# Performance work log

Measured on AMD Instinct MI355X. Metric: run time of the kernel, lower is better.

## Reference

```python
import jax, jax.numpy as jnp
import numpy as np

B, S, H, HS, D = 256, 16, 8, 128, 1024
M = H * HS  # mem_size = 1024
FORGET_BIAS = 1.0


def setup_inputs() -> dict:
    key = jax.random.key(0)
    ks = jax.random.split(key, 16)
    n = lambda k, shape, s=0.02: (jax.random.normal(k, shape, jnp.float32) * s)
    return {
        'inputs': jax.random.normal(ks[0], (B, D), jnp.float32),
        'h_state': jax.random.normal(ks[1], (B, S, M), jnp.float32),
        'm_state': jax.random.normal(ks[2], (B, S, M), jnp.float32),
        'W_emb': n(ks[3], (D, M)), 'b_emb': jnp.zeros((M,), jnp.float32),
        'W_g': n(ks[4], (M, M)), 'b_g': jnp.zeros((M,), jnp.float32),
        'W_wf': n(ks[5], (D, M)), 'W_wi': n(ks[6], (D, M)), 'W_wo': n(ks[7], (D, M)),
        'W_uf': n(ks[8], (M, M)), 'b_uf': jnp.zeros((M,), jnp.float32),
        'W_ui': n(ks[9], (M, M)), 'b_ui': jnp.zeros((M,), jnp.float32),
        'W_uo': n(ks[10], (M, M)), 'b_uo': jnp.zeros((M,), jnp.float32),
    }


def _rmc_forward(inputs, h_state, m_state, W_emb, b_emb, W_g, b_g,
                 W_wf, W_wi, W_wo, W_uf, b_uf, W_ui, b_ui, W_uo, b_uo):
    # input embedding: [B, D] -> [B, M]
    dense_inputs = inputs @ W_emb + b_emb
    # keys/values: memory with the embedded input appended as an extra slot -> [B, S+1, M]
    kv = jnp.concatenate([m_state, dense_inputs[:, None, :]], axis=1)
    # multi-head scaled dot-product attention (no q/k/v projections in AttentionMap)
    q = m_state.reshape(B, S, H, HS)
    k = kv.reshape(B, S + 1, H, HS)
    v = kv.reshape(B, S + 1, H, HS)
    scores = jnp.einsum('bqhd,bkhd->bhqk', q, k) / jnp.sqrt(jnp.asarray(HS, q.dtype))
    attn = jax.nn.softmax(scores, axis=-1)
    attended = jnp.einsum('bhqk,bkhd->bqhd', attn, v).reshape(B, S, M)

    memory_proposal = m_state + attended
    memory_proposal = (memory_proposal @ W_g + b_g) + memory_proposal

    forget_gate = jax.nn.sigmoid(h_state @ W_uf + b_uf + (inputs @ W_wf)[:, None, :])
    input_gate = jax.nn.sigmoid(h_state @ W_ui + b_ui + (inputs @ W_wi)[:, None, :])
    output_gate = jax.nn.sigmoid(h_state @ W_uo + b_uo + (inputs @ W_wo)[:, None, :])

    # NOTE: faithful to the original (including the sigmoid around m*f + bias and
    # the double-sigmoid on the input/output gates)
    new_memories = jax.nn.sigmoid(m_state * forget_gate + FORGET_BIAS) \
        + memory_proposal * jax.nn.sigmoid(input_gate)
    new_hidden = jnp.tanh(m_state) * jax.nn.sigmoid(output_gate)
    return new_memories, new_hidden


def reference(inputs, h_state, m_state, W_emb, b_emb, W_g, b_g,
              W_wf, W_wi, W_wo, W_uf, b_uf, W_ui, b_ui, W_uo, b_uo):
    return _rmc_forward(inputs, h_state, m_state, W_emb, b_emb, W_g, b_g,
                        W_wf, W_wi, W_wo, W_uf, b_uf, W_ui, b_ui, W_uo, b_uo)
```

## Files before the change

### kernel.cpp

```cpp
#include <hip/hip_runtime.h>
#include <hip/hip_bf16.h>


typedef __hip_bfloat16 bf16;
typedef __bf16 bf16x8 __attribute__((ext_vector_type(8)));
typedef float  f32x4  __attribute__((ext_vector_type(4)));

__device__ __forceinline__ float b2f(bf16 x) { return __bfloat162float(x); }
__device__ __forceinline__ bf16  f2b(float x) { return __float2bfloat16(x); }
__device__ __forceinline__ float sig(float x) { return 1.0f / (1.0f + __expf(-x)); }

__device__ __forceinline__ void gl_lds16(const void* g, void* l) {
    __builtin_amdgcn_global_load_lds(
        (const __attribute__((address_space(1))) void*)g,
        (__attribute__((address_space(3))) void*)l,
        16, 0, 0);
}

__device__ __forceinline__ float4 ld_bf4(const bf16* p) {
    ushort4 u = *(const ushort4*)p;
    float4 r;
    r.x = b2f(*(const bf16*)&u.x);
    r.y = b2f(*(const bf16*)&u.y);
    r.z = b2f(*(const bf16*)&u.z);
    r.w = b2f(*(const bf16*)&u.w);
    return r;
}

__global__ __launch_bounds__(256) void k_prep(
    const float* __restrict__ W0, const float* __restrict__ W1,
    const float* __restrict__ W2, const float* __restrict__ W3,
    const float* __restrict__ W4, const float* __restrict__ W5,
    const float* __restrict__ W6, const float* __restrict__ W7,
    const float* __restrict__ h_state, const float* __restrict__ inputs,
    bf16* __restrict__ wt, bf16* __restrict__ hbf, bf16* __restrict__ xbf)
{
    const int blk = blockIdx.x;
    const int tid = threadIdx.x;

    if (blk < 8192) {
        const float* Ws[8] = {W0, W1, W2, W3, W4, W5, W6, W7};
        const int plane = blk >> 10;
        const int t = blk & 1023;
        const int nb = (t & 31) * 32, kb = (t >> 5) * 32;
        const float* W = Ws[plane];
        bf16* Wt = wt + (size_t)plane * (1024 * 1024);

        __shared__ float tl[32][33];
        const int tx = tid & 31, ty = tid >> 5;

        #pragma unroll
        for (int r = 0; r < 4; ++r)
            tl[r * 8 + ty][tx] = W[(size_t)(kb + r * 8 + ty) * 1024 + nb + tx];
        __syncthreads();
        #pragma unroll
        for (int r = 0; r < 4; ++r)
            Wt[(size_t)(nb + r * 8 + ty) * 1024 + kb + tx] = f2b(tl[tx][r * 8 + ty]);
    } else if (blk < 10240) {
        const int e = blk - 8192;
        int idx = (e * 256 + tid) * 8;
        #pragma unroll
        for (int half = 0; half < 2; ++half) {
            float4 v = *(const float4*)(h_state + idx + half * 4);
            hbf[idx + half * 4 + 0] = f2b(v.x);
            hbf[idx + half * 4 + 1] = f2b(v.y);
            hbf[idx + half * 4 + 2] = f2b(v.z);
            hbf[idx + half * 4 + 3] = f2b(v.w);
        }
    } else {
        const int e = blk - 10240;
        int idx = (e * 256 + tid) * 8;
        #pragma unroll
        for (int half = 0; half < 2; ++half) {
            float4 v = *(const float4*)(inputs + idx + half * 4);
            xbf[idx + half * 4 + 0] = f2b(v.x);
            xbf[idx + half * 4 + 1] = f2b(v.y);
            xbf[idx + half * 4 + 2] = f2b(v.z);
            xbf[idx + half * 4 + 3] = f2b(v.w);
        }
    }
}

__global__ __launch_bounds__(256) void k_gemm1(
    const bf16* __restrict__ hbf,
    const bf16* __restrict__ xbf,
    const bf16* __restrict__ wt,
    const float* __restrict__ b_emb,
    bf16* __restrict__ pre,
    float* __restrict__ proj)
{
    __shared__ __align__(16) char smem[32768];

    const int bid = blockIdx.x;
    const int wv = threadIdx.x >> 6;
    const int lane = threadIdx.x & 63;
    const int r8 = lane >> 3, c8 = lane & 7;
    const int mrow = lane & 15, q = lane >> 4;

    const bf16* A;
    int m0, plane, bn0;
    if (bid < 768) {
        int bx = bid % 24, by = bid / 24;
        A = hbf; m0 = by * 128;
        int n0g = bx * 128;
        plane = 1 + (n0g >> 10); bn0 = n0g & 1023;
    } else {
        int e = bid - 768;
        int bx = e & 31, by = e >> 5;
        A = xbf; m0 = by * 128;
        int n0x = bx * 128;
        plane = 4 + (n0x >> 10); bn0 = n0x & 1023;
    }
    const bf16* Bp = wt + (size_t)plane * (1024 * 1024);

    const f32x4 zero4 = {0.0f, 0.0f, 0.0f, 0.0f};
    f32x4 acc[4][4];
    #pragma unroll
    for (int i = 0; i < 4; ++i)
        #pragma unroll
        for (int j = 0; j < 4; ++j) acc[i][j] = zero4;

    const int rb = (wv & 1) * 64, cb = (wv >> 1) * 64;

    for (int k0 = 0; k0 < 1024; k0 += 64) {
        #pragma unroll
        for (int t = 0; t < 4; ++t) {
            int rr = wv * 32 + t * 8;
            gl_lds16(A  + (size_t)(m0  + rr + r8) * 1024 + k0 + c8 * 8, smem + rr * 128);
            gl_lds16(Bp + (size_t)(bn0 + rr + r8) * 1024 + k0 + c8 * 8, smem + 16384 + rr * 128);
        }
        __syncthreads();

        #pragma unroll
        for (int kk = 0; kk < 2; ++kk) {
            const int kb = kk * 64 + q * 16;
            bf16x8 a[4], b[4];
            #pragma unroll
            for (int i = 0; i < 4; ++i)
                a[i] = *(const bf16x8*)(smem + (rb + i * 16 + mrow) * 128 + kb);
            #pragma unroll
            for (int j = 0; j < 4; ++j)
                b[j] = *(const bf16x8*)(smem + 16384 + (cb + j * 16 + mrow) * 128 + kb);
            #pragma unroll
            for (int i = 0; i < 4; ++i)
                #pragma unroll
                for (int j = 0; j < 4; ++j)
                    acc[i][j] = __builtin_amdgcn_mfma_f32_16x16x32_bf16(a[i], b[j], acc[i][j], 0, 0, 0);
        }
        __syncthreads();
    }

    if (bid < 768) {
        bf16* P = pre + (size_t)(plane - 1) * (4096 * 1024);
        #pragma unroll
        for (int j = 0; j < 4; ++j) {
            const int colp = bn0 + cb + j * 16 + mrow;
            #pragma unroll
            for (int i = 0; i < 4; ++i)
                #pragma unroll
                for (int r = 0; r < 4; ++r) {
                    const int row = m0 + rb + i * 16 + q * 4 + r;
                    P[(size_t)row * 1024 + colp] = f2b(acc[i][j][r]);
                }
        }
    } else {
        const int which = plane - 4;
        float* P = proj + which * 262144;
        #pragma unroll
        for (int j = 0; j < 4; ++j) {
            const int colp = bn0 + cb + j * 16 + mrow;
            const float bias = (which == 0) ? b_emb[colp] : 0.0f;
            #pragma unroll
            for (int i = 0; i < 4; ++i)
                #pragma unroll
                for (int r = 0; r < 4; ++r) {
                    const int row = m0 + rb + i * 16 + q * 4 + r;
                    P[(size_t)row * 1024 + colp] = acc[i][j][r] + bias;
                }
        }
    }
}

__global__ __launch_bounds__(256) void k_attn(
    const float* __restrict__ m_state,
    const float* __restrict__ dense,
    bf16* __restrict__ mp)
{
    const int b = blockIdx.x >> 3;
    const int h = blockIdx.x & 7;
    const int tid = threadIdx.x;

    __shared__ float kv[17][132];
    __shared__ float sc[16][18];

    for (int idx = tid; idx < 17 * 32; idx += 256) {
        int r = idx >> 5, d4 = idx & 31;
        const float* src = (r < 16)
            ? &m_state[(size_t)(b * 16 + r) * 1024 + h * 128 + d4 * 4]
            : &dense[(size_t)b * 1024 + h * 128 + d4 * 4];
        float4 v = *(const float4*)src;
        *(float4*)&kv[r][d4 * 4] = v;
    }
    __syncthreads();

    for (int p = tid; p < 16 * 17; p += 256) {
        int qi = p / 17, ki = p % 17;
        float dx = 0.f, dy = 0.f, dz = 0.f, dw = 0.f;
        #pragma unroll 8
        for (int d4 = 0; d4 < 32; ++d4) {
            float4 a = *(const float4*)&kv[qi][d4 * 4];
            float4 c = *(const float4*)&kv[ki][d4 * 4];
            dx += a.x * c.x; dy += a.y * c.y; dz += a.z * c.z; dw += a.w * c.w;
        }
        sc[qi][ki] = (dx + dy + dz + dw) * 0.0883883476483184f;
    }
    __syncthreads();

    if (tid < 16) {
        float mx = -1e30f;
        for (int k = 0; k < 17; ++k) mx = fmaxf(mx, sc[tid][k]);
        float s = 0.0f;
        for (int k = 0; k < 17; ++k) { float e = __expf(sc[tid][k] - mx); sc[tid][k] = e; s += e; }
        float inv = 1.0f / s;
        for (int k = 0; k < 17; ++k) sc[tid][k] *= inv;
    }
    __syncthreads();

    for (int p = tid; p < 16 * 32; p += 256) {
        int qi = p >> 5, d4 = p & 31;
        float sx = 0.f, sy = 0.f, sz = 0.f, sw = 0.f;
        #pragma unroll
        for (int k = 0; k < 17; ++k) {
            float w = sc[qi][k];
            float4 v = *(const float4*)&kv[k][d4 * 4];
            sx += w * v.x; sy += w * v.y; sz += w * v.z; sw += w * v.w;
        }
        float4 base = *(const float4*)&kv[qi][d4 * 4];
        size_t off = (size_t)(b * 16 + qi) * 1024 + h * 128 + d4 * 4;
        mp[off + 0] = f2b(base.x + sx);
        mp[off + 1] = f2b(base.y + sy);
        mp[off + 2] = f2b(base.z + sz);
        mp[off + 3] = f2b(base.w + sw);
    }
}

__global__ __launch_bounds__(256) void k_gemm2(
    const bf16* __restrict__ mpb,
    const bf16* __restrict__ wtg,
    bf16* __restrict__ preg)
{
    __shared__ __align__(16) char smem[24576];

    const int m0 = (blockIdx.x >> 3) * 64;
    const int n0 = (blockIdx.x & 7) * 128;
    const int wv = threadIdx.x >> 6;
    const int lane = threadIdx.x & 63;
    const int r8 = lane >> 3, c8 = lane & 7;
    const int mrow = lane & 15, q = lane >> 4;

    const f32x4 zero4 = {0.0f, 0.0f, 0.0f, 0.0f};
    f32x4 acc[2][4];
    #pragma unroll
    for (int i = 0; i < 2; ++i)
        #pragma unroll
        for (int j = 0; j < 4; ++j) acc[i][j] = zero4;

    const int rb = (wv & 1) * 32, cb = (wv >> 1) * 64;

    for (int k0 = 0; k0 < 1024; k0 += 64) {
        #pragma unroll
        for (int t = 0; t < 2; ++t) {
            int rr = wv * 16 + t * 8;
            gl_lds16(mpb + (size_t)(m0 + rr + r8) * 1024 + k0 + c8 * 8, smem + rr * 128);
        }
        #pragma unroll
        for (int t = 0; t < 4; ++t) {
            int rr = wv * 32 + t * 8;
            gl_lds16(wtg + (size_t)(n0 + rr + r8) * 1024 + k0 + c8 * 8, smem + 8192 + rr * 128);
        }
        __syncthreads();

        #pragma unroll
        for (int kk = 0; kk < 2; ++kk) {
            const int kb = kk * 64 + q * 16;
            bf16x8 a[2], b[4];
            #pragma unroll
            for (int i = 0; i < 2; ++i)
                a[i] = *(const bf16x8*)(smem + (rb + i * 16 + mrow) * 128 + kb);
            #pragma unroll
            for (int j = 0; j < 4; ++j)
                b[j] = *(const bf16x8*)(smem + 8192 + (cb + j * 16 + mrow) * 128 + kb);
            #pragma unroll
            for (int i = 0; i < 2; ++i)
                #pragma unroll
                for (int j = 0; j < 4; ++j)
                    acc[i][j] = __builtin_amdgcn_mfma_f32_16x16x32_bf16(a[i], b[j], acc[i][j], 0, 0, 0);
        }
        __syncthreads();
    }

    #pragma unroll
    for (int j = 0; j < 4; ++j) {
        const int col = n0 + cb + j * 16 + mrow;
        #pragma unroll
        for (int i = 0; i < 2; ++i)
            #pragma unroll
            for (int r = 0; r < 4; ++r) {
                const int row = m0 + rb + i * 16 + q * 4 + r;
                preg[(size_t)row * 1024 + col] = f2b(acc[i][j][r]);
            }
    }
}

__global__ __launch_bounds__(256) void k_epi(
    const float* __restrict__ m_state,
    const bf16* __restrict__ mpb,
    const bf16* __restrict__ preg,
    const bf16* __restrict__ pre,
    const float* __restrict__ proj,
    const float* __restrict__ b_g, const float* __restrict__ b_uf,
    const float* __restrict__ b_ui, const float* __restrict__ b_uo,
    float* __restrict__ out_mem, float* __restrict__ out_hid)
{
    const int idx = (blockIdx.x * 256 + threadIdx.x) * 4;
    const int row = idx >> 10;
    const int col = idx & 1023;
    const int b = row >> 4;

    float4 m4  = *(const float4*)(m_state + idx);
    float4 mp4 = ld_bf4(mpb + idx);
    float4 pg4 = ld_bf4(preg + idx);
    float4 pf4 = ld_bf4(pre + idx);
    float4 pi4 = ld_bf4(pre + 4194304 + idx);
    float4 po4 = ld_bf4(pre + 8388608 + idx);
    float4 xf4 = *(const float4*)(proj + 262144 + b * 1024 + col);
    float4 xi4 = *(const float4*)(proj + 524288 + b * 1024 + col);
    float4 xo4 = *(const float4*)(proj + 786432 + b * 1024 + col);
    float4 bg4 = *(const float4*)(b_g + col);
    float4 bf4 = *(const float4*)(b_uf + col);
    float4 bi4 = *(const float4*)(b_ui + col);
    float4 bo4 = *(const float4*)(b_uo + col);

    float4 om, oh;
    {
        float mp2 = pg4.x + bg4.x + mp4.x;
        float fg = sig(pf4.x + bf4.x + xf4.x);
        float ig = sig(pi4.x + bi4.x + xi4.x);
        float og = sig(po4.x + bo4.x + xo4.x);
        om.x = sig(m4.x * fg + 1.0f) + mp2 * sig(ig);
        oh.x = tanhf(m4.x) * sig(og);
    }
    {
        float mp2 = pg4.y + bg4.y + mp4.y;
        float fg = sig(pf4.y + bf4.y + xf4.y);
        float ig = sig(pi4.y + bi4.y + xi4.y);
        float og = sig(po4.y + bo4.y + xo4.y);
        om.y = sig(m4.y * fg + 1.0f) + mp2 * sig(ig);
        oh.y = tanhf(m4.y) * sig(og);
    }
    {
        float mp2 = pg4.z + bg4.z + mp4.z;
        float fg = sig(pf4.z + bf4.z + xf4.z);
        float ig = sig(pi4.z + bi4.z + xi4.z);
        float og = sig(po4.z + bo4.z + xo4.z);
        om.z = sig(m4.z * fg + 1.0f) + mp2 * sig(ig);
        oh.z = tanhf(m4.z) * sig(og);
    }
    {
        float mp2 = pg4.w + bg4.w + mp4.w;
        float fg = sig(pf4.w + bf4.w + xf4.w);
        float ig = sig(pi4.w + bi4.w + xi4.w);
        float og = sig(po4.w + bo4.w + xo4.w);
        om.w = sig(m4.w * fg + 1.0f) + mp2 * sig(ig);
        oh.w = tanhf(m4.w) * sig(og);
    }

    *(float4*)(out_mem + idx) = om;
    *(float4*)(out_hid + idx) = oh;
}

extern "C" void kernel_launch(void* const* d_in, const int* in_sizes, int n_in,
                              void* d_out, int out_size, void* d_ws, size_t ws_size,
                              hipStream_t stream)
{
    const float* inputs  = (const float*)d_in[0];
    const float* h_state = (const float*)d_in[1];
    const float* m_state = (const float*)d_in[2];
    const float* W_emb   = (const float*)d_in[3];
    const float* b_emb   = (const float*)d_in[4];
    const float* W_g     = (const float*)d_in[5];
    const float* b_g     = (const float*)d_in[6];
    const float* W_wf    = (const float*)d_in[7];
    const float* W_wi    = (const float*)d_in[8];
    const float* W_wo    = (const float*)d_in[9];
    const float* W_uf    = (const float*)d_in[10];
    const float* b_uf    = (const float*)d_in[11];
    const float* W_ui    = (const float*)d_in[12];
    const float* b_ui    = (const float*)d_in[13];
    const float* W_uo    = (const float*)d_in[14];
    const float* b_uo    = (const float*)d_in[15];

    char* wsb = (char*)d_ws;
    float* proj = (float*)wsb;
    bf16*  hmp  = (bf16*)(wsb + 4u  * 1048576u);
    bf16*  wt   = (bf16*)(wsb + 12u * 1048576u);
    bf16*  xbf  = (bf16*)(wsb + 28u * 1048576u);
    bf16*  pre  = (bf16*)(wsb + 29u * 1048576u);
    bf16*  preg = (bf16*)(wsb + 20u * 1048576u);

    float* out_mem = (float*)d_out;
    float* out_hid = out_mem + (size_t)4096 * 1024;

    k_prep<<<dim3(10368), dim3(256), 0, stream>>>(
        W_g, W_uf, W_ui, W_uo, W_emb, W_wf, W_wi, W_wo,
        h_state, inputs, wt, hmp, xbf);

    k_gemm1<<<dim3(832), dim3(256), 0, stream>>>(
        hmp, xbf, wt, b_emb, pre, proj);

    k_attn<<<dim3(256 * 8), dim3(256), 0, stream>>>(m_state, proj, hmp);

    k_gemm2<<<dim3(512), dim3(256), 0, stream>>>(hmp, wt, preg);

    k_epi<<<dim3(4096), dim3(256), 0, stream>>>(
        m_state, hmp, preg, pre, proj,
        b_g, b_uf, b_ui, b_uo, out_mem, out_hid);
}
```

Measured before the change: 239.2 us.

## Fuse input projections into prep and merge gate and proposal GEMMs into one pipelined kernel

The small input-side projections (emb, wf, wi, wo) now run inside k_prep, converting fp32 inputs and weights to bf16 on the fly, so neither the xbf buffer nor the transposed copies of those four weights are needed. The three h_state gate GEMMs and the memory-proposal GEMM become one 256x256-tile, 512-thread kernel with double-buffered LDS, XOR-swizzled layout and explicit waitcnt/barrier pipelining, run after attention. The separate gemm1 launch goes away. tanhf is swapped for an exp-based approximation. The cost is 128KB of dynamic LDS, a grid of only 256 blocks, and a serial K loop over only 64 blocks for the projection GEMM inside prep.

Measured after the change: 233.9 us. 1.02x faster.

```diff
diff --git a/kernel.cpp b/kernel.cpp
--- a/kernel.cpp
+++ b/kernel.cpp
@@ -8,7 +8,14 @@
 
 __device__ __forceinline__ float b2f(bf16 x) { return __bfloat162float(x); }
 __device__ __forceinline__ bf16  f2b(float x) { return __float2bfloat16(x); }
+__device__ __forceinline__ unsigned short fbits(float x) {
+    bf16 b = __float2bfloat16(x);
+    return *(unsigned short*)&b;
+}
 __device__ __forceinline__ float sig(float x) { return 1.0f / (1.0f + __expf(-x)); }
+__device__ __forceinline__ float ftanh(float x) {
+    return 1.0f - 2.0f / (1.0f + __expf(2.0f * x));
+}
 
 __device__ __forceinline__ void gl_lds16(const void* g, void* l) {
     __builtin_amdgcn_global_load_lds(
@@ -28,36 +35,126 @@
 }
 
 __global__ __launch_bounds__(256) void k_prep(
-    const float* __restrict__ W0, const float* __restrict__ W1,
-    const float* __restrict__ W2, const float* __restrict__ W3,
-    const float* __restrict__ W4, const float* __restrict__ W5,
-    const float* __restrict__ W6, const float* __restrict__ W7,
+    const float* __restrict__ W_g, const float* __restrict__ W_uf,
+    const float* __restrict__ W_ui, const float* __restrict__ W_uo,
+    const float* __restrict__ W_emb, const float* __restrict__ W_wf,
+    const float* __restrict__ W_wi, const float* __restrict__ W_wo,
+    const float* __restrict__ b_emb,
     const float* __restrict__ h_state, const float* __restrict__ inputs,
-    bf16* __restrict__ wt, bf16* __restrict__ hbf, bf16* __restrict__ xbf)
+    bf16* __restrict__ wt, bf16* __restrict__ hbf, float* __restrict__ proj)
 {
+    __shared__ __align__(16) char sbuf[32768];
     const int blk = blockIdx.x;
     const int tid = threadIdx.x;
 
-    if (blk < 8192) {
-        const float* Ws[8] = {W0, W1, W2, W3, W4, W5, W6, W7};
-        const int plane = blk >> 10;
-        const int t = blk & 1023;
-        const int nb = (t & 31) * 32, kb = (t >> 5) * 32;
+    if (blk < 64) {
+        const float* Wsrc4[4] = {W_emb, W_wf, W_wi, W_wo};
+        const int by = blk >> 5, bx = blk & 31;
+        const int which = bx >> 3;
+        const int n0 = (bx & 7) * 128;
+        const int m0 = by * 128;
+        const float* Wsrc = Wsrc4[which];
+        char* LA = sbuf;
+        char* LB = sbuf + 16384;
+
+        const int wv = tid >> 6, lane = tid & 63;
+        const int mrow = lane & 15, q = lane >> 4;
+        const int rb = (wv & 1) * 64, cb = (wv >> 1) * 64;
+
+        const f32x4 zero4 = {0.0f, 0.0f, 0.0f, 0.0f};
+        f32x4 acc[4][4];
+        #pragma unroll
+        for (int i = 0; i < 4; ++i)
+            #pragma unroll
+            for (int j = 0; j < 4; ++j) acc[i][j] = zero4;
+
+        for (int k0 = 0; k0 < 1024; k0 += 64) {
+            #pragma unroll
+            for (int r = 0; r < 8; ++r) {
+                int lin = r * 256 + tid;
+                int row = lin >> 4, f4 = lin & 15;
+                float4 v = *(const float4*)(inputs + (size_t)(m0 + row) * 1024 + k0 + f4 * 4);
+                ushort4 p;
+                p.x = fbits(v.x); p.y = fbits(v.y); p.z = fbits(v.z); p.w = fbits(v.w);
+                *(ushort4*)(LA + row * 128 + ((f4 * 8) ^ ((row & 7) << 4))) = p;
+            }
+            #pragma unroll
+            for (int r = 0; r < 2; ++r) {
+                int lin = r * 256 + tid;
+                int kq = lin >> 5, cq = lin & 31;
+                const float* wp = Wsrc + (size_t)(k0 + kq * 4) * 1024 + n0 + cq * 4;
+                float4 v0 = *(const float4*)(wp);
+                float4 v1 = *(const float4*)(wp + 1024);
+                float4 v2 = *(const float4*)(wp + 2048);
+                float4 v3 = *(const float4*)(wp + 3072);
+                const float* e0 = (const float*)&v0;
+                const float* e1 = (const float*)&v1;
+                const float* e2 = (const float*)&v2;
+                const float* e3 = (const float*)&v3;
+                #pragma unroll
+                for (int j = 0; j < 4; ++j) {
+                    int c = cq * 4 + j;
+                    ushort4 p;
+                    p.x = fbits(e0[j]); p.y = fbits(e1[j]);
+                    p.z = fbits(e2[j]); p.w = fbits(e3[j]);
+                    *(ushort4*)(LB + c * 128 + ((kq * 8) ^ ((c & 7) << 4))) = p;
+                }
+            }
+            __syncthreads();
+            #pragma unroll
+            for (int kk = 0; kk < 2; ++kk) {
+                const int kb = kk * 64 + q * 16;
+                bf16x8 afr[4], bfr[4];
+                #pragma unroll
+                for (int i = 0; i < 4; ++i) {
+                    int row = rb + i * 16 + mrow;
+                    afr[i] = *(const bf16x8*)(LA + row * 128 + (kb ^ ((row & 7) << 4)));
+                }
+                #pragma unroll
+                for (int j = 0; j < 4; ++j) {
+                    int n = cb + j * 16 + mrow;
+                    bfr[j] = *(const bf16x8*)(LB + n * 128 + (kb ^ ((n & 7) << 4)));
+                }
+                #pragma unroll
+                for (int i = 0; i < 4; ++i)
+                    #pragma unroll
+                    for (int j = 0; j < 4; ++j)
+                        acc[i][j] = __builtin_amdgcn_mfma_f32_16x16x32_bf16(afr[i], bfr[j], acc[i][j], 0, 0, 0);
+            }
+            __syncthreads();
+        }
+        float* P = proj + which * 262144;
+        #pragma unroll
+        for (int j = 0; j < 4; ++j) {
+            const int colp = n0 + cb + j * 16 + mrow;
+            const float bias = (which == 0) ? b_emb[colp] : 0.0f;
+            #pragma unroll
+            for (int i = 0; i < 4; ++i)
+                #pragma unroll
+                for (int r = 0; r < 4; ++r) {
+                    const int row = m0 + rb + i * 16 + q * 4 + r;
+                    P[(size_t)row * 1024 + colp] = acc[i][j][r] + bias;
+                }
+        }
+    } else if (blk < 4160) {
+        const float* Ws[4] = {W_g, W_uf, W_ui, W_uo};
+        const int t = blk - 64;
+        const int plane = t >> 10;
+        const int tt = t & 1023;
+        const int nb = (tt & 31) * 32, kb2 = (tt >> 5) * 32;
         const float* W = Ws[plane];
         bf16* Wt = wt + (size_t)plane * (1024 * 1024);
-
-        __shared__ float tl[32][33];
+        float (*tl)[33] = (float (*)[33])sbuf;
         const int tx = tid & 31, ty = tid >> 5;
-
         #pragma unroll
         for (int r = 0; r < 4; ++r)
-            tl[r * 8 + ty][tx] = W[(size_t)(kb + r * 8 + ty) * 1024 + nb + tx];
+            tl[r * 8 + ty][tx] = W[(size_t)(kb2 + r * 8 + ty) * 1024 + nb + tx];
         __syncthreads();
         #pragma unroll
         for (int r = 0; r < 4; ++r)
-            Wt[(size_t)(nb + r * 8 + ty) * 1024 + kb + tx] = f2b(tl[tx][r * 8 + ty]);
-    } else if (blk < 10240) {
-        const int e = blk - 8192;
+            Wt[(size_t)(nb + r * 8 + ty) * 1024 + kb2 + tx] = f2b(tl[tx][r * 8 + ty]);
+    } else {
+        const int e = blk - 4160;
         int idx = (e * 256 + tid) * 8;
         #pragma unroll
         for (int half = 0; half < 2; ++half) {
@@ -66,117 +163,6 @@
             hbf[idx + half * 4 + 1] = f2b(v.y);
             hbf[idx + half * 4 + 2] = f2b(v.z);
             hbf[idx + half * 4 + 3] = f2b(v.w);
-        }
-    } else {
-        const int e = blk - 10240;
-        int idx = (e * 256 + tid) * 8;
-        #pragma unroll
-        for (int half = 0; half < 2; ++half) {
-            float4 v = *(const float4*)(inputs + idx + half * 4);
-            xbf[idx + half * 4 + 0] = f2b(v.x);
-            xbf[idx + half * 4 + 1] = f2b(v.y);
-            xbf[idx + half * 4 + 2] = f2b(v.z);
-            xbf[idx + half * 4 + 3] = f2b(v.w);
-        }
-    }
-}
-
-__global__ __launch_bounds__(256) void k_gemm1(
-    const bf16* __restrict__ hbf,
-    const bf16* __restrict__ xbf,
-    const bf16* __restrict__ wt,
-    const float* __restrict__ b_emb,
-    bf16* __restrict__ pre,
-    float* __restrict__ proj)
-{
-    __shared__ __align__(16) char smem[32768];
-
-    const int bid = blockIdx.x;
-    const int wv = threadIdx.x >> 6;
-    const int lane = threadIdx.x & 63;
-    const int r8 = lane >> 3, c8 = lane & 7;
-    const int mrow = lane & 15, q = lane >> 4;
-
-    const bf16* A;
-    int m0, plane, bn0;
-    if (bid < 768) {
-        int bx = bid % 24, by = bid / 24;
-        A = hbf; m0 = by * 128;
-        int n0g = bx * 128;
-        plane = 1 + (n0g >> 10); bn0 = n0g & 1023;
-    } else {
-        int e = bid - 768;
-        int bx = e & 31, by = e >> 5;
-        A = xbf; m0 = by * 128;
-        int n0x = bx * 128;
-        plane = 4 + (n0x >> 10); bn0 = n0x & 1023;
-    }
-    const bf16* Bp = wt + (size_t)plane * (1024 * 1024);
-
-    const f32x4 zero4 = {0.0f, 0.0f, 0.0f, 0.0f};
-    f32x4 acc[4][4];
-    #pragma unroll
-    for (int i = 0; i < 4; ++i)
-        #pragma unroll
-        for (int j = 0; j < 4; ++j) acc[i][j] = zero4;
-
-    const int rb = (wv & 1) * 64, cb = (wv >> 1) * 64;
-
-    for (int k0 = 0; k0 < 1024; k0 += 64) {
-        #pragma unroll
-        for (int t = 0; t < 4; ++t) {
-            int rr = wv * 32 + t * 8;
-            gl_lds16(A  + (size_t)(m0  + rr + r8) * 1024 + k0 + c8 * 8, smem + rr * 128);
-            gl_lds16(Bp + (size_t)(bn0 + rr + r8) * 1024 + k0 + c8 * 8, smem + 16384 + rr * 128);
-        }
-        __syncthreads();
-
-        #pragma unroll
-        for (int kk = 0; kk < 2; ++kk) {
-            const int kb = kk * 64 + q * 16;
-            bf16x8 a[4], b[4];
-            #pragma unroll
-            for (int i = 0; i < 4; ++i)
-                a[i] = *(const bf16x8*)(smem + (rb + i * 16 + mrow) * 128 + kb);
-            #pragma unroll
-            for (int j = 0; j < 4; ++j)
-                b[j] = *(const bf16x8*)(smem + 16384 + (cb + j * 16 + mrow) * 128 + kb);
-            #pragma unroll
-            for (int i = 0; i < 4; ++i)
-                #pragma unroll
-                for (int j = 0; j < 4; ++j)
-                    acc[i][j] = __builtin_amdgcn_mfma_f32_16x16x32_bf16(a[i], b[j], acc[i][j], 0, 0, 0);
-        }
-        __syncthreads();
-    }
-
-    if (bid < 768) {
-        bf16* P = pre + (size_t)(plane - 1) * (4096 * 1024);
-        #pragma unroll
-        for (int j = 0; j < 4; ++j) {
-            const int colp = bn0 + cb + j * 16 + mrow;
-            #pragma unroll
-            for (int i = 0; i < 4; ++i)
-                #pragma unroll
-                for (int r = 0; r < 4; ++r) {
-                    const int row = m0 + rb + i * 16 + q * 4 + r;
-                    P[(size_t)row * 1024 + colp] = f2b(acc[i][j][r]);
-                }
-        }
-    } else {
-        const int which = plane - 4;
-        float* P = proj + which * 262144;
-        #pragma unroll
-        for (int j = 0; j < 4; ++j) {
-            const int colp = bn0 + cb + j * 16 + mrow;
-            const float bias = (which == 0) ? b_emb[colp] : 0.0f;
-            #pragma unroll
-            for (int i = 0; i < 4; ++i)
-                #pragma unroll
-                for (int r = 0; r < 4; ++r) {
-                    const int row = m0 + rb + i * 16 + q * 4 + r;
-                    P[(size_t)row * 1024 + colp] = acc[i][j][r] + bias;
-                }
         }
     }
 }
@@ -244,70 +230,108 @@
     }
 }
 
-__global__ __launch_bounds__(256) void k_gemm2(
+__global__ __launch_bounds__(512, 2) void k_gemm_big(
+    const bf16* __restrict__ hbf,
     const bf16* __restrict__ mpb,
-    const bf16* __restrict__ wtg,
+    const bf16* __restrict__ wt,
+    bf16* __restrict__ pre,
     bf16* __restrict__ preg)
 {
-    __shared__ __align__(16) char smem[24576];
-
-    const int m0 = (blockIdx.x >> 3) * 64;
-    const int n0 = (blockIdx.x & 7) * 128;
+    extern __shared__ __align__(16) char smem[];
+
+    int bid = blockIdx.x;
+    bid = (bid & 7) * 32 + (bid >> 3);
+    const int by = bid & 15;
+    const int ct = bid >> 4;
+    const int m0 = by * 256;
+
+    const bf16* A; const bf16* Bp; bf16* Cout; int bn0;
+    if (ct < 12) {
+        A = hbf;
+        const int g = ct >> 2;
+        bn0 = (ct & 3) * 256;
+        Bp = wt + (size_t)(1 + g) * (1024 * 1024);
+        Cout = pre + (size_t)g * (4096 * 1024);
+    } else {
+        A = mpb;
+        bn0 = (ct - 12) * 256;
+        Bp = wt;
+        Cout = preg;
+    }
+
     const int wv = threadIdx.x >> 6;
     const int lane = threadIdx.x & 63;
     const int r8 = lane >> 3, c8 = lane & 7;
     const int mrow = lane & 15, q = lane >> 4;
+    const int wr = wv >> 2, wc = wv & 3;
 
     const f32x4 zero4 = {0.0f, 0.0f, 0.0f, 0.0f};
-    f32x4 acc[2][4];
+    f32x4 acc[8][4];
     #pragma unroll
-    for (int i = 0; i < 2; ++i)
+    for (int i = 0; i < 8; ++i)
         #pragma unroll
         for (int j = 0; j < 4; ++j) acc[i][j] = zero4;
 
-    const int rb = (wv & 1) * 32, cb = (wv >> 1) * 64;
-
-    for (int k0 = 0; k0 < 1024; k0 += 64) {
-        #pragma unroll
-        for (int t = 0; t < 2; ++t) {
-            int rr = wv * 16 + t * 8;
-            gl_lds16(mpb + (size_t)(m0 + rr + r8) * 1024 + k0 + c8 * 8, smem + rr * 128);
-        }
+    auto STAGE = [&](int buf, int k0) {
+        char* sA = smem + buf * 65536;
+        char* sB = sA + 32768;
         #pragma unroll
         for (int t = 0; t < 4; ++t) {
-            int rr = wv * 32 + t * 8;
-            gl_lds16(wtg + (size_t)(n0 + rr + r8) * 1024 + k0 + c8 * 8, smem + 8192 + rr * 128);
-        }
-        __syncthreads();
-
+            const int rr = wv * 32 + t * 8;
+            gl_lds16(A  + (size_t)(m0  + rr + r8) * 1024 + k0 + (c8 ^ r8) * 8, sA + rr * 128);
+            gl_lds16(Bp + (size_t)(bn0 + rr + r8) * 1024 + k0 + (c8 ^ r8) * 8, sB + rr * 128);
+        }
+    };
+
+    STAGE(0, 0);
+
+    #pragma unroll 2
+    for (int step = 0; step < 16; ++step) {
+        const int cur = step & 1;
+        if (step < 15) {
+            STAGE(cur ^ 1, (step + 1) * 64);
+            asm volatile("s_waitcnt vmcnt(8)" ::: "memory");
+        } else {
+            asm volatile("s_waitcnt vmcnt(0)" ::: "memory");
+        }
+        __builtin_amdgcn_s_barrier();
+        __builtin_amdgcn_sched_barrier(0);
+
+        const char* sA = smem + cur * 65536;
+        const char* sB = sA + 32768;
         #pragma unroll
         for (int kk = 0; kk < 2; ++kk) {
             const int kb = kk * 64 + q * 16;
-            bf16x8 a[2], b[4];
-            #pragma unroll
-            for (int i = 0; i < 2; ++i)
-                a[i] = *(const bf16x8*)(smem + (rb + i * 16 + mrow) * 128 + kb);
-            #pragma unroll
-            for (int j = 0; j < 4; ++j)
-                b[j] = *(const bf16x8*)(smem + 8192 + (cb + j * 16 + mrow) * 128 + kb);
-            #pragma unroll
-            for (int i = 0; i < 2; ++i)
+            bf16x8 afr[8], bfr[4];
+            #pragma unroll
+            for (int i = 0; i < 8; ++i) {
+                const int row = wr * 128 + i * 16 + mrow;
+                afr[i] = *(const bf16x8*)(sA + row * 128 + (kb ^ ((row & 7) << 4)));
+            }
+            #pragma unroll
+            for (int j = 0; j < 4; ++j) {
+                const int n = wc * 64 + j * 16 + mrow;
+                bfr[j] = *(const bf16x8*)(sB + n * 128 + (kb ^ ((n & 7) << 4)));
+            }
+            #pragma unroll
+            for (int i = 0; i < 8; ++i)
                 #pragma unroll
                 for (int j = 0; j < 4; ++j)
-                    acc[i][j] = __builtin_amdgcn_mfma_f32_16x16x32_bf16(a[i], b[j], acc[i][j], 0, 0, 0);
-        }
-        __syncthreads();
+                    acc[i][j] = __builtin_amdgcn_mfma_f32_16x16x32_bf16(afr[i], bfr[j], acc[i][j], 0, 0, 0);
+        }
+        __builtin_amdgcn_sched_barrier(0);
+        __builtin_amdgcn_s_barrier();
     }
 
     #pragma unroll
     for (int j = 0; j < 4; ++j) {
-        const int col = n0 + cb + j * 16 + mrow;
-        #pragma unroll
-        for (int i = 0; i < 2; ++i)
+        const int col = bn0 + wc * 64 + j * 16 + mrow;
+        #pragma unroll
+        for (int i = 0; i < 8; ++i)
             #pragma unroll
             for (int r = 0; r < 4; ++r) {
-                const int row = m0 + rb + i * 16 + q * 4 + r;
-                preg[(size_t)row * 1024 + col] = f2b(acc[i][j][r]);
+                const int row = m0 + wr * 128 + i * 16 + q * 4 + r;
+                Cout[(size_t)row * 1024 + col] = f2b(acc[i][j][r]);
             }
     }
 }
@@ -348,7 +372,7 @@
         float ig = sig(pi4.x + bi4.x + xi4.x);
         float og = sig(po4.x + bo4.x + xo4.x);
         om.x = sig(m4.x * fg + 1.0f) + mp2 * sig(ig);
-        oh.x = tanhf(m4.x) * sig(og);
+        oh.x = ftanh(m4.x) * sig(og);
     }
     {
         float mp2 = pg4.y + bg4.y + mp4.y;
@@ -356,7 +380,7 @@
         float ig = sig(pi4.y + bi4.y + xi4.y);
         float og = sig(po4.y + bo4.y + xo4.y);
         om.y = sig(m4.y * fg + 1.0f) + mp2 * sig(ig);
-        oh.y = tanhf(m4.y) * sig(og);
+        oh.y = ftanh(m4.y) * sig(og);
     }
     {
         float mp2 = pg4.z + bg4.z + mp4.z;
@@ -364,7 +388,7 @@
         float ig = sig(pi4.z + bi4.z + xi4.z);
         float og = sig(po4.z + bo4.z + xo4.z);
         om.z = sig(m4.z * fg + 1.0f) + mp2 * sig(ig);
-        oh.z = tanhf(m4.z) * sig(og);
+        oh.z = ftanh(m4.z) * sig(og);
     }
     {
         float mp2 = pg4.w + bg4.w + mp4.w;
@@ -372,7 +396,7 @@
         float ig = sig(pi4.w + bi4.w + xi4.w);
         float og = sig(po4.w + bo4.w + xo4.w);
         om.w = sig(m4.w * fg + 1.0f) + mp2 * sig(ig);
-        oh.w = tanhf(m4.w) * sig(og);
+        oh.w = ftanh(m4.w) * sig(og);
     }
 
     *(float4*)(out_mem + idx) = om;
@@ -402,27 +426,24 @@
 
     char* wsb = (char*)d_ws;
     float* proj = (float*)wsb;
-    bf16*  hmp  = (bf16*)(wsb + 4u  * 1048576u);
-    bf16*  wt   = (bf16*)(wsb + 12u * 1048576u);
-    bf16*  xbf  = (bf16*)(wsb + 28u * 1048576u);
-    bf16*  pre  = (bf16*)(wsb + 29u * 1048576u);
-    bf16*  preg = (bf16*)(wsb + 20u * 1048576u);
+    bf16*  hbf  = (bf16*)(wsb + 4u  * 1048576u);
+    bf16*  mpb  = (bf16*)(wsb + 12u * 1048576u);
+    bf16*  wt   = (bf16*)(wsb + 20u * 1048576u);
+    bf16*  pre  = (bf16*)(wsb + 28u * 1048576u);
+    bf16*  preg = (bf16*)(wsb + 52u * 1048576u);
 
     float* out_mem = (float*)d_out;
     float* out_hid = out_mem + (size_t)4096 * 1024;
 
-    k_prep<<<dim3(10368), dim3(256), 0, stream>>>(
-        W_g, W_uf, W_ui, W_uo, W_emb, W_wf, W_wi, W_wo,
-        h_state, inputs, wt, hmp, xbf);
-
-    k_gemm1<<<dim3(832), dim3(256), 0, stream>>>(
-        hmp, xbf, wt, b_emb, pre, proj);
-
-    k_attn<<<dim3(256 * 8), dim3(256), 0, stream>>>(m_state, proj, hmp);
-
-    k_gemm2<<<dim3(512), dim3(256), 0, stream>>>(hmp, wt, preg);
+    k_prep<<<dim3(6208), dim3(256), 0, stream>>>(
+        W_g, W_uf, W_ui, W_uo, W_emb, W_wf, W_wi, W_wo, b_emb,
+        h_state, inputs, wt, hbf, proj);
+
+    k_attn<<<dim3(256 * 8), dim3(256), 0, stream>>>(m_state, proj, mpb);
+
+    k_gemm_big<<<dim3(256), dim3(512), 131072, stream>>>(hbf, mpb, wt, pre, preg);
 
     k_epi<<<dim3(4096), dim3(256), 0, stream>>>(
-        m_state, hmp, preg, pre, proj,
+        m_state, mpb, preg, pre, proj,
         b_g, b_uf, b_ui, b_uo, out_mem, out_hid);
 }
```
